# Performance work log

Hardware: AMD Instinct MI355X
Metric: run time of the kernel (lower is better)

The kernel has to match this reference:

```python
import jax, jax.numpy as jnp
import numpy as np

ARITY = 4  # matches init_kwargs; params.shape[1] == 2**ARITY


def _high_order_act(X, params):
    # X: [B, G*arity], params: [G, 2**arity, O]
    B = X.shape[0]
    G, _, O = params.shape
    a = ARITY
    A = X.reshape(B, G, a)
    # sort ascending along the arity dim (torch.sort returns values + indices)
    A_ind = jnp.argsort(A, axis=2)                      # [B, G, a] int32
    A_sort = jnp.take_along_axis(A, A_ind, axis=2)      # [B, G, a]
    # barycentric-style coefficients: smallest value, then successive diffs
    coef = jnp.concatenate(
        [A_sort[:, :, :1], A_sort[:, :, 1:] - A_sort[:, :, :-1]], axis=2
    )                                                   # [B, G, a]
    # bit-power index: reverse cumsum of 2**A_ind -> suffix sums of bit masks
    pow2 = jnp.left_shift(jnp.int32(1), A_ind.astype(jnp.int32))  # [B, G, a]
    idx = jnp.cumsum(pow2[:, :, ::-1], axis=2)[:, :, ::-1]        # [B, G, a], in [1, 2**a - 1]
    # gather per-group table rows: params[g, idx[b,g,k], :]
    g_idx = jnp.arange(G)[None, :, None]                # [1, G, 1]
    gathered = params[g_idx, idx]                       # [B, G, a, O]
    # einsum 'jikl,ijk->ijl' in torch (j=G, i=B) == 'bgao,bga->bgo' here
    out = jnp.einsum('bgao,bga->bgo', gathered, coef)   # [B, G, O]
    return out.reshape(B, G * O)


def setup_inputs() -> dict:
    key = jax.random.key(0)
    kx, kp = jax.random.split(key)
    B, G, a, O = 8192, 256, ARITY, 16
    X = jax.random.normal(kx, (B, G * a), dtype=jnp.float32)
    params = jax.random.normal(kp, (G, 2 ** a, O), dtype=jnp.float32)
    return {"X": X, "params": params}


def reference(X, params):
    return _high_order_act(X, params)
```

## Files before the change

kernel.cpp:

```cpp
#include <hip/hip_runtime.h>


typedef float f32x4 __attribute__((ext_vector_type(4)));

#define NT 1024
#define TG 64
#define ROWS 64
#define WPB 16
#define TSTRIDE 260

__device__ __forceinline__ void row_compute_store(
    f32x4 x, const float* tab, int key, float* obase)
{
    float v0 = x.x, v1 = x.y, v2 = x.z, v3 = x.w;
    int i0 = 0, i1 = 1, i2 = 2, i3 = 3;

#define CSWAP(va, vb, ia, ib)                         \
    {                                                 \
        bool sw_ = (va) > (vb);                       \
        float lo_ = sw_ ? (vb) : (va);                \
        float hi_ = sw_ ? (va) : (vb);                \
        int il_ = sw_ ? (ib) : (ia);                  \
        int ih_ = sw_ ? (ia) : (ib);                  \
        (va) = lo_; (vb) = hi_; (ia) = il_; (ib) = ih_; \
    }
    CSWAP(v0, v1, i0, i1);
    CSWAP(v2, v3, i2, i3);
    CSWAP(v0, v2, i0, i2);
    CSWAP(v1, v3, i1, i3);
    CSWAP(v1, v2, i1, i2);
#undef CSWAP

    float c0 = v0, c1 = v1 - v0, c2 = v2 - v1, c3 = v3 - v2;
    int idx0 = 15;
    int idx1 = 15 ^ (1 << i0);
    int idx2 = idx1 ^ (1 << i1);
    int idx3 = 1 << i3;

#pragma unroll
    for (int k = 0; k < 4; ++k) {
        f32x4 A  = *reinterpret_cast<const f32x4*>(tab + 4 * ((idx0 * 4 + k) ^ key));
        f32x4 Bv = *reinterpret_cast<const f32x4*>(tab + 4 * ((idx1 * 4 + k) ^ key));
        f32x4 C  = *reinterpret_cast<const f32x4*>(tab + 4 * ((idx2 * 4 + k) ^ key));
        f32x4 D  = *reinterpret_cast<const f32x4*>(tab + 4 * ((idx3 * 4 + k) ^ key));
        f32x4 o;
        o.x = fmaf(c3, D.x, fmaf(c2, C.x, fmaf(c1, Bv.x, c0 * A.x)));
        o.y = fmaf(c3, D.y, fmaf(c2, C.y, fmaf(c1, Bv.y, c0 * A.y)));
        o.z = fmaf(c3, D.z, fmaf(c2, C.z, fmaf(c1, Bv.z, c0 * A.z)));
        o.w = fmaf(c3, D.w, fmaf(c2, C.w, fmaf(c1, Bv.w, c0 * A.w)));
        *reinterpret_cast<f32x4*>(obase + k * 4) = o;
    }
}

__global__ __launch_bounds__(NT, 4) void hoa_kernel(
    const float* __restrict__ X, const float* __restrict__ P,
    float* __restrict__ out, int B, int G)
{
    __shared__ float lds[TG * TSTRIDE];

    const int tid = threadIdx.x;
    const int g0 = blockIdx.x * TG;
    const int b0 = blockIdx.y * ROWS;

#pragma unroll
    for (int i = 0; i < (TG * 64) / NT; ++i) {
        int idx = tid + i * NT;
        int t = idx >> 6;
        int w = idx & 63;
        f32x4 v = *reinterpret_cast<const f32x4*>(
            P + (size_t)(g0 + t) * 256 + w * 4);
        int ws = w ^ ((t >> 3) & 7);
        *reinterpret_cast<f32x4*>(&lds[t * TSTRIDE + ws * 4]) = v;
    }
    __syncthreads();

    const int gg = tid & 63;
    const int wv = tid >> 6;
    const int g  = g0 + gg;
    const float* tab = &lds[gg * TSTRIDE];
    const int key = (gg >> 3) & 7;

    const int r0 = b0 + wv;
    const int r1 = r0 + WPB, r2 = r1 + WPB, r3 = r2 + WPB;

    f32x4 x0, x1, x2, x3;
    if (r0 < B) x0 = *reinterpret_cast<const f32x4*>(X + (size_t)r0 * (G * 4) + g * 4);
    if (r1 < B) x1 = *reinterpret_cast<const f32x4*>(X + (size_t)r1 * (G * 4) + g * 4);
    if (r2 < B) x2 = *reinterpret_cast<const f32x4*>(X + (size_t)r2 * (G * 4) + g * 4);
    if (r3 < B) x3 = *reinterpret_cast<const f32x4*>(X + (size_t)r3 * (G * 4) + g * 4);

    if (r0 < B) row_compute_store(x0, tab, key, out + (size_t)r0 * (G * 16) + (size_t)g * 16);
    if (r1 < B) row_compute_store(x1, tab, key, out + (size_t)r1 * (G * 16) + (size_t)g * 16);
    if (r2 < B) row_compute_store(x2, tab, key, out + (size_t)r2 * (G * 16) + (size_t)g * 16);
    if (r3 < B) row_compute_store(x3, tab, key, out + (size_t)r3 * (G * 16) + (size_t)g * 16);
}

extern "C" void kernel_launch(void* const* d_in, const int* in_sizes, int n_in,
                              void* d_out, int out_size, void* d_ws, size_t ws_size,
                              hipStream_t stream) {
    const float* X = (const float*)d_in[0];
    const float* P = (const float*)d_in[1];
    float* out = (float*)d_out;

    int G = in_sizes[1] / 256;
    int B = in_sizes[0] / (G * 4);

    dim3 grid(G / TG, (B + ROWS - 1) / ROWS);
    hipLaunchKernelGGL(hoa_kernel, grid, dim3(NT), 0, stream, X, P, out, B, G);
}
```

Measured before the change: 176.0 us.

## Split each group's output across four lanes for contiguous coalesced stores

Remaps threads so that four adjacent lanes share one group and each computes one float4 chunk of the 16-wide output. A wave now writes contiguous 256-byte runs instead of 64-byte strided chunks per lane, which should improve store coalescing. Each lane now redundantly loads and sorts the X quad, and the row loop processes four consecutive rows per wave. The LDS XOR swizzle is removed and occupancy bounds are lowered to 2, which may cause LDS bank conflicts and lower occupancy.

```diff
diff --git a/kernel.cpp b/kernel.cpp
--- a/kernel.cpp
+++ b/kernel.cpp
@@ -5,12 +5,11 @@
 
 #define NT 1024
 #define TG 64
-#define ROWS 64
-#define WPB 16
+#define RPW 4
+#define ROWS (16 * RPW)
 #define TSTRIDE 260
 
-__device__ __forceinline__ void row_compute_store(
-    f32x4 x, const float* tab, int key, float* obase)
+__device__ __forceinline__ f32x4 one_chunk(f32x4 x, const float* tab)
 {
     float v0 = x.x, v1 = x.y, v2 = x.z, v3 = x.w;
     int i0 = 0, i1 = 1, i2 = 2, i3 = 3;
@@ -37,22 +36,20 @@
     int idx2 = idx1 ^ (1 << i1);
     int idx3 = 1 << i3;
 
-#pragma unroll
-    for (int k = 0; k < 4; ++k) {
-        f32x4 A  = *reinterpret_cast<const f32x4*>(tab + 4 * ((idx0 * 4 + k) ^ key));
-        f32x4 Bv = *reinterpret_cast<const f32x4*>(tab + 4 * ((idx1 * 4 + k) ^ key));
-        f32x4 C  = *reinterpret_cast<const f32x4*>(tab + 4 * ((idx2 * 4 + k) ^ key));
-        f32x4 D  = *reinterpret_cast<const f32x4*>(tab + 4 * ((idx3 * 4 + k) ^ key));
-        f32x4 o;
-        o.x = fmaf(c3, D.x, fmaf(c2, C.x, fmaf(c1, Bv.x, c0 * A.x)));
-        o.y = fmaf(c3, D.y, fmaf(c2, C.y, fmaf(c1, Bv.y, c0 * A.y)));
-        o.z = fmaf(c3, D.z, fmaf(c2, C.z, fmaf(c1, Bv.z, c0 * A.z)));
-        o.w = fmaf(c3, D.w, fmaf(c2, C.w, fmaf(c1, Bv.w, c0 * A.w)));
-        *reinterpret_cast<f32x4*>(obase + k * 4) = o;
-    }
+    f32x4 A  = *reinterpret_cast<const f32x4*>(tab + idx0 * 16);
+    f32x4 Bv = *reinterpret_cast<const f32x4*>(tab + idx1 * 16);
+    f32x4 C  = *reinterpret_cast<const f32x4*>(tab + idx2 * 16);
+    f32x4 D  = *reinterpret_cast<const f32x4*>(tab + idx3 * 16);
+
+    f32x4 o;
+    o.x = fmaf(c3, D.x, fmaf(c2, C.x, fmaf(c1, Bv.x, c0 * A.x)));
+    o.y = fmaf(c3, D.y, fmaf(c2, C.y, fmaf(c1, Bv.y, c0 * A.y)));
+    o.z = fmaf(c3, D.z, fmaf(c2, C.z, fmaf(c1, Bv.z, c0 * A.z)));
+    o.w = fmaf(c3, D.w, fmaf(c2, C.w, fmaf(c1, Bv.w, c0 * A.w)));
+    return o;
 }
 
-__global__ __launch_bounds__(NT, 4) void hoa_kernel(
+__global__ __launch_bounds__(NT, 2) void hoa_kernel(
     const float* __restrict__ X, const float* __restrict__ P,
     float* __restrict__ out, int B, int G)
 {
@@ -69,30 +66,41 @@
         int w = idx & 63;
         f32x4 v = *reinterpret_cast<const f32x4*>(
             P + (size_t)(g0 + t) * 256 + w * 4);
-        int ws = w ^ ((t >> 3) & 7);
-        *reinterpret_cast<f32x4*>(&lds[t * TSTRIDE + ws * 4]) = v;
+        *reinterpret_cast<f32x4*>(&lds[t * TSTRIDE + w * 4]) = v;
     }
     __syncthreads();
 
-    const int gg = tid & 63;
-    const int wv = tid >> 6;
-    const int g  = g0 + gg;
-    const float* tab = &lds[gg * TSTRIDE];
-    const int key = (gg >> 3) & 7;
+    const int c    = tid & 3;
+    const int gg16 = (tid >> 2) & 15;
+    const int wv   = tid >> 6;
 
-    const int r0 = b0 + wv;
-    const int r1 = r0 + WPB, r2 = r1 + WPB, r3 = r2 + WPB;
+    const float* tabq0 = &lds[(0 * 16 + gg16) * TSTRIDE + c * 4];
+    const float* tabq1 = &lds[(1 * 16 + gg16) * TSTRIDE + c * 4];
+    const float* tabq2 = &lds[(2 * 16 + gg16) * TSTRIDE + c * 4];
+    const float* tabq3 = &lds[(3 * 16 + gg16) * TSTRIDE + c * 4];
 
-    f32x4 x0, x1, x2, x3;
-    if (r0 < B) x0 = *reinterpret_cast<const f32x4*>(X + (size_t)r0 * (G * 4) + g * 4);
-    if (r1 < B) x1 = *reinterpret_cast<const f32x4*>(X + (size_t)r1 * (G * 4) + g * 4);
-    if (r2 < B) x2 = *reinterpret_cast<const f32x4*>(X + (size_t)r2 * (G * 4) + g * 4);
-    if (r3 < B) x3 = *reinterpret_cast<const f32x4*>(X + (size_t)r3 * (G * 4) + g * 4);
+#pragma unroll
+    for (int rr = 0; rr < RPW; ++rr) {
+        const int r = b0 + wv * RPW + rr;
+        if (r >= B) break;
 
-    if (r0 < B) row_compute_store(x0, tab, key, out + (size_t)r0 * (G * 16) + (size_t)g * 16);
-    if (r1 < B) row_compute_store(x1, tab, key, out + (size_t)r1 * (G * 16) + (size_t)g * 16);
-    if (r2 < B) row_compute_store(x2, tab, key, out + (size_t)r2 * (G * 16) + (size_t)g * 16);
-    if (r3 < B) row_compute_store(x3, tab, key, out + (size_t)r3 * (G * 16) + (size_t)g * 16);
+        const float* xrow = X   + (size_t)r * (G * 4)  + g0 * 4;
+        float*       orow = out + (size_t)r * (G * 16) + (size_t)g0 * 16;
+
+        f32x4 xq0 = *reinterpret_cast<const f32x4*>(xrow + (0 * 16 + gg16) * 4);
+        f32x4 xq1 = *reinterpret_cast<const f32x4*>(xrow + (1 * 16 + gg16) * 4);
+        f32x4 xq2 = *reinterpret_cast<const f32x4*>(xrow + (2 * 16 + gg16) * 4);
+        f32x4 xq3 = *reinterpret_cast<const f32x4*>(xrow + (3 * 16 + gg16) * 4);
+
+        f32x4 o0 = one_chunk(xq0, tabq0);
+        *reinterpret_cast<f32x4*>(orow + ((0 * 16 + gg16) * 16) + c * 4) = o0;
+        f32x4 o1 = one_chunk(xq1, tabq1);
+        *reinterpret_cast<f32x4*>(orow + ((1 * 16 + gg16) * 16) + c * 4) = o1;
+        f32x4 o2 = one_chunk(xq2, tabq2);
+        *reinterpret_cast<f32x4*>(orow + ((2 * 16 + gg16) * 16) + c * 4) = o2;
+        f32x4 o3 = one_chunk(xq3, tabq3);
+        *reinterpret_cast<f32x4*>(orow + ((3 * 16 + gg16) * 16) + c * 4) = o3;
+    }
 }
 
 extern "C" void kernel_launch(void* const* d_in, const int* in_sizes, int n_in,
```

Result: faster. 166.7 us (-5.3%).
